# Optimization experiments

Hardware: AMD Instinct MI355X
Metric: run time of the kernel (lower is better)

The kernel has to match this reference:

```python
import jax, jax.numpy as jnp
import numpy as np

TOPK = 4  # constructor default topk=4


def setup_inputs() -> dict:
    key = jax.random.key(0)
    k_x, k_a, k_b, k_w, k_bias = jax.random.split(key, 5)
    b, s, h, j, a, r = 4, 2048, 2048, 2048, 64, 16
    x = jax.random.normal(k_x, (b, s, h), dtype=jnp.float32)
    A = jax.random.normal(k_a, (a, r, h), dtype=jnp.float32) * 0.02   # adapter down-proj bank
    B = jax.random.normal(k_b, (a, j, r), dtype=jnp.float32) * 0.02   # adapter up-proj bank
    W = jax.random.normal(k_w, (j, h), dtype=jnp.float32) * 0.02      # base Linear weight
    bias = jax.random.normal(k_bias, (j,), dtype=jnp.float32) * 0.02  # base Linear bias
    return {"x": x, "A": A, "B": B, "W": W, "bias": bias}


def reference(x, A, B, W, bias):
    # vecs: per-adapter low-rank projections of each token. [b,s,a,r]
    vecs = jnp.einsum('arh,bsh->bsar', A, x)
    # routing score = L2 norm over rank dim. [b,s,a]
    arrows = jnp.linalg.norm(vecs, axis=-1)
    # top-k adapters per token -> uniform 1/topk routing weights (scatter of a constant,
    # so no gradient flows through the routing weights, matching torch semantics).
    _, idx = jax.lax.top_k(arrows, TOPK)                     # [b,s,topk]
    routes = jax.nn.one_hot(idx, arrows.shape[-1], dtype=x.dtype).sum(-2) / TOPK  # [b,s,a]
    # weighted combine of selected adapter vecs. [b,s,r]
    v = jnp.einsum('bsa,bsar->bsr', routes, vecs)
    # delta = (routes-weighted B) applied to v; contract over a then r without
    # materializing the [b,s,j,r] intermediate. [b,s,j]
    delta = jnp.einsum('bsa,ajr,bsr->bsj', routes, B, v)
    base = jnp.einsum('bsh,jh->bsj', x, W) + bias
    return base + delta
```

## Files before the change

### kernel.cpp

```cpp
#include <hip/hip_runtime.h>
#include <hip/hip_bf16.h>
#include <stdint.h>

#define TOKENS 8192
#define H 2048
#define JDIM 2048
#define NADAPT 64
#define RANK 16
#define KG 1024
#define KTOT 3072
#define NT2 48

typedef __bf16 v8bf __attribute__((ext_vector_type(8)));
typedef float v4f __attribute__((ext_vector_type(4)));
typedef unsigned short us8 __attribute__((ext_vector_type(8)));
typedef unsigned short us4 __attribute__((ext_vector_type(4)));

__device__ __forceinline__ unsigned short f2bf(float f) {
  union { __bf16 b; unsigned short u; } c; c.b = (__bf16)f; return c.u;
}
__device__ __forceinline__ float bf2f(unsigned short u) {
  union { unsigned int u; float f; } c; c.u = ((unsigned int)u) << 16; return c.f;
}

__device__ __forceinline__ us8 pack8(float4 a, float4 b) {
  us8 r;
  r[0]=f2bf(a.x); r[1]=f2bf(a.y); r[2]=f2bf(a.z); r[3]=f2bf(a.w);
  r[4]=f2bf(b.x); r[5]=f2bf(b.y); r[6]=f2bf(b.z); r[7]=f2bf(b.w);
  return r;
}

__device__ __forceinline__ void split8(float4 a, float4 b, us8& h, us8& l) {
  float v[8] = {a.x, a.y, a.z, a.w, b.x, b.y, b.z, b.w};
  #pragma unroll
  for (int i = 0; i < 8; ++i) {
    h[i] = f2bf(v[i]);
    l[i] = f2bf(v[i] - bf2f(h[i]));
  }
}

__global__ void cast_x_split_kernel(const float* __restrict__ x,
                                    unsigned short* __restrict__ XG,
                                    unsigned short* __restrict__ XLO) {
  int idx = blockIdx.x * 256 + threadIdx.x;
  int row = idx >> 8;
  int cg  = idx & 255;
  const float4* s = (const float4*)(x + ((size_t)row << 11) + ((size_t)cg << 3));
  float4 a = s[0], b = s[1];
  us8 h, l;
  split8(a, b, h, l);
  *(us8*)(XG  + (size_t)row * KTOT + ((size_t)cg << 3)) = h;
  *(us8*)(XLO + (size_t)row * H    + ((size_t)cg << 3)) = l;
}

__global__ void cast_a_split_kernel(const float* __restrict__ A,
                                    unsigned short* __restrict__ Ahi,
                                    unsigned short* __restrict__ Alo) {
  int idx = blockIdx.x * 256 + threadIdx.x;
  int row = idx >> 8;
  int cg  = idx & 255;
  const float4* s = (const float4*)(A + ((size_t)row << 11) + ((size_t)cg << 3));
  float4 a = s[0], b = s[1];
  us8 h, l;
  split8(a, b, h, l);
  *(us8*)(Ahi + (size_t)row * H + ((size_t)cg << 3)) = h;
  *(us8*)(Alo + (size_t)row * H + ((size_t)cg << 3)) = l;
}

__global__ void cast2048_kernel(const float* __restrict__ src,
                                unsigned short* __restrict__ dst, int dstld) {
  int idx = blockIdx.x * 256 + threadIdx.x;
  int row = idx >> 8;
  int cg  = idx & 255;
  const float4* s = (const float4*)(src + ((size_t)row << 11) + ((size_t)cg << 3));
  float4 a = s[0], b = s[1];
  *(us8*)(dst + (size_t)row * dstld + ((size_t)cg << 3)) = pack8(a, b);
}

__global__ void cast_b_kernel(const float* __restrict__ Bsrc,
                              unsigned short* __restrict__ WB) {
  int idx = blockIdx.x * 256 + threadIdx.x;
  int a = idx >> 11, j = idx & 2047;
  const float4* s = (const float4*)(Bsrc + (((size_t)a << 11) + j) * RANK);
  float4 f0 = s[0], f1 = s[1], f2 = s[2], f3 = s[3];
  us8* d = (us8*)(WB + (size_t)j * KTOT + H + a * RANK);
  d[0] = pack8(f0, f1);
  d[1] = pack8(f2, f3);
}

__global__ void route_kernel(const float* __restrict__ vecs,
                             unsigned short* __restrict__ XG) {
  __shared__ float vsh[4][16];
  int wave = threadIdx.x >> 6, lane = threadIdx.x & 63;
  int t = blockIdx.x * 4 + wave;
  const float* vrow = vecs + (size_t)t * KG;
  const float4* vp = (const float4*)(vrow + lane * RANK);
  float4 q0 = vp[0], q1 = vp[1], q2 = vp[2], q3 = vp[3];
  float ss = q0.x*q0.x + q0.y*q0.y + q0.z*q0.z + q0.w*q0.w
           + q1.x*q1.x + q1.y*q1.y + q1.z*q1.z + q1.w*q1.w
           + q2.x*q2.x + q2.y*q2.y + q2.z*q2.z + q2.w*q2.w
           + q3.x*q3.x + q3.y*q3.y + q3.z*q3.z + q3.w*q3.w;
  float arr = ss;
  int sel[4];
  #pragma unroll
  for (int k = 0; k < 4; ++k) {
    float m = arr; int mi = lane;
    #pragma unroll
    for (int o = 32; o > 0; o >>= 1) {
      float om = __shfl_xor(m, o);
      int oi  = __shfl_xor(mi, o);
      if (om > m || (om == m && oi < mi)) { m = om; mi = oi; }
    }
    sel[k] = mi;
    if (lane == mi) arr = -3.0e38f;
  }
  if (lane < 16) {
    float s = vrow[sel[0]*RANK + lane] + vrow[sel[1]*RANK + lane]
            + vrow[sel[2]*RANK + lane] + vrow[sel[3]*RANK + lane];
    vsh[wave][lane] = 0.0625f * s;
  }
  __syncthreads();
  bool on = (lane == sel[0]) | (lane == sel[1]) | (lane == sel[2]) | (lane == sel[3]);
  us8 lo, hi;
  #pragma unroll
  for (int r = 0; r < 8; ++r) lo[r] = on ? f2bf(vsh[wave][r])     : (unsigned short)0;
  #pragma unroll
  for (int r = 0; r < 8; ++r) hi[r] = on ? f2bf(vsh[wave][r + 8]) : (unsigned short)0;
  us8* d = (us8*)(XG + (size_t)t * KTOT + H + lane * RANK);
  d[0] = lo; d[1] = hi;
}

__device__ __forceinline__ void gload_lds16(const void* gsrc, void* ldst) {
  __builtin_amdgcn_global_load_lds(
      (const __attribute__((address_space(1))) unsigned int*)gsrc,
      (__attribute__((address_space(3))) unsigned int*)ldst, 16, 0, 0);
}

__global__ __launch_bounds__(256, 2) void gemm1_kernel(
    const unsigned short* __restrict__ Xhi,
    const unsigned short* __restrict__ Xlo,
    const unsigned short* __restrict__ Ahi,
    const unsigned short* __restrict__ Alo,
    float* __restrict__ C) {
  __shared__ unsigned short AsH[128 * 32];
  __shared__ unsigned short AsL[128 * 32];
  __shared__ unsigned short BsH[128 * 32];
  __shared__ unsigned short BsL[128 * 32];
  const int tid = threadIdx.x;
  const int lane = tid & 63, wave = tid >> 6;
  const int wr = wave >> 1, wc = wave & 1;
  const int bm = blockIdx.x, bn = blockIdx.y;

  v4f acc[4][4];
  #pragma unroll
  for (int i = 0; i < 4; ++i)
    #pragma unroll
    for (int j = 0; j < 4; ++j)
      acc[i][j] = (v4f){0.f, 0.f, 0.f, 0.f};

  const unsigned short* XhiB = Xhi + (size_t)(bm * 128) * KTOT;
  const unsigned short* XloB = Xlo + (size_t)(bm * 128) * H;
  const unsigned short* AhiB = Ahi + (size_t)(bn * 128) * H;
  const unsigned short* AloB = Alo + (size_t)(bn * 128) * H;

  const int rA = lane & 15;
  const int kkx = (((lane >> 4) ^ ((rA >> 1) & 3)) << 3);

  for (int k0 = 0; k0 < H; k0 += 32) {
    #pragma unroll
    for (int rnd = 0; rnd < 2; ++rnd) {
      int e = rnd * 256 + tid;
      int r = e >> 2;
      int c8 = (((e & 3) ^ ((e >> 3) & 3)) << 3);
      gload_lds16(XhiB + (size_t)r * KTOT + k0 + c8, (char*)AsH + (size_t)e * 16);
      gload_lds16(XloB + (size_t)r * H    + k0 + c8, (char*)AsL + (size_t)e * 16);
      gload_lds16(AhiB + (size_t)r * H    + k0 + c8, (char*)BsH + (size_t)e * 16);
      gload_lds16(AloB + (size_t)r * H    + k0 + c8, (char*)BsL + (size_t)e * 16);
    }
    __syncthreads();
    v8bf ah[4], al[4], bh[4], bl[4];
    #pragma unroll
    for (int i = 0; i < 4; ++i) {
      ah[i] = *(const v8bf*)&AsH[(wr * 64 + i * 16 + rA) * 32 + kkx];
      al[i] = *(const v8bf*)&AsL[(wr * 64 + i * 16 + rA) * 32 + kkx];
    }
    #pragma unroll
    for (int j = 0; j < 4; ++j) {
      bh[j] = *(const v8bf*)&BsH[(wc * 64 + j * 16 + rA) * 32 + kkx];
      bl[j] = *(const v8bf*)&BsL[(wc * 64 + j * 16 + rA) * 32 + kkx];
    }
    #pragma unroll
    for (int i = 0; i < 4; ++i)
      #pragma unroll
      for (int j = 0; j < 4; ++j) {
        acc[i][j] = __builtin_amdgcn_mfma_f32_16x16x32_bf16(ah[i], bh[j], acc[i][j], 0, 0, 0);
        acc[i][j] = __builtin_amdgcn_mfma_f32_16x16x32_bf16(ah[i], bl[j], acc[i][j], 0, 0, 0);
        acc[i][j] = __builtin_amdgcn_mfma_f32_16x16x32_bf16(al[i], bh[j], acc[i][j], 0, 0, 0);
      }
    __syncthreads();
  }

  const int rowbase = bm * 128 + wr * 64;
  const int colbase = bn * 128 + wc * 64;
  #pragma unroll
  for (int i = 0; i < 4; ++i) {
    int r0 = rowbase + i * 16 + ((lane >> 4) << 2);
    #pragma unroll
    for (int j = 0; j < 4; ++j) {
      int col = colbase + j * 16 + (lane & 15);
      #pragma unroll
      for (int q = 0; q < 4; ++q)
        C[(size_t)(r0 + q) * KG + col] = acc[i][j][q];
    }
  }
}

#define BAR() asm volatile("s_waitcnt lgkmcnt(0)\n\ts_barrier" ::: "memory")
#define VM8() asm volatile("s_waitcnt vmcnt(8)" ::: "memory")

#define STAGE(regionUS, panel, kelem) do {                                        \
  gload_lds16((panel) + aoff0 + (kelem), (char*)(regionUS) + tid * 16);           \
  gload_lds16((panel) + aoff1 + (kelem), (char*)(regionUS) + 8192 + tid * 16);    \
} while (0)

#define PHASE(mh, RAr, RBr, ISSUE, DOVM) do {                                     \
  if ((mh) == 0) {                                                                \
    _Pragma("unroll")                                                             \
    for (int j = 0; j < 4; ++j)                                                   \
      bfr[j] = *(const v8bf*)((const char*)(RBr) + bbyte + j * 1024);             \
  }                                                                               \
  _Pragma("unroll")                                                               \
  for (int i = 0; i < 4; ++i)                                                     \
    af[i] = *(const v8bf*)((const char*)(RAr) + abyte + ((mh)*4 + i) * 1024);     \
  ISSUE;                                                                          \
  BAR();                                                                          \
  __builtin_amdgcn_s_setprio(1);                                                  \
  _Pragma("unroll")                                                               \
  for (int i = 0; i < 4; ++i)                                                     \
    _Pragma("unroll")                                                             \
    for (int j = 0; j < 4; ++j)                                                   \
      acc[(mh)*4 + i][j] = __builtin_amdgcn_mfma_f32_16x16x32_bf16(               \
          af[i], bfr[j], acc[(mh)*4 + i][j], 0, 0, 0);                            \
  __builtin_amdgcn_s_setprio(0);                                                  \
  DOVM;                                                                           \
  BAR();                                                                          \
} while (0)

__global__ __launch_bounds__(512, 1) void gemm2_8ph_kernel(
    const unsigned short* __restrict__ Xg, const unsigned short* __restrict__ Wb,
    float* __restrict__ C, const float* __restrict__ bias) {
  __shared__ unsigned short lds[65536];
  const int tid = threadIdx.x;
  const int lane = tid & 63, wid = tid >> 6;
  const int wr = wid >> 2, wc = wid & 3;
  const int rA = lane & 15, grp = lane >> 4;
  const int grpx = (grp ^ ((rA >> 1) & 3)) << 4;

  const int bid = blockIdx.x;
  const int bn = bid & 7, bm = bid >> 3;

  const unsigned short* Ap = Xg + (size_t)(bm * 256) * KTOT;
  const unsigned short* Bp = Wb + (size_t)(bn * 256) * KTOT;

  const int srow = tid >> 2;
  const int scol = ((tid & 3) ^ ((tid >> 3) & 3)) << 3;
  const size_t aoff0 = (size_t)srow * KTOT + scol;
  const size_t aoff1 = (size_t)(srow + 128) * KTOT + scol;

  unsigned short* A0k0 = lds;
  unsigned short* A0k1 = lds + 8192;
  unsigned short* B0k0 = lds + 16384;
  unsigned short* B0k1 = lds + 24576;
  unsigned short* A1k0 = lds + 32768;
  unsigned short* A1k1 = lds + 40960;
  unsigned short* B1k0 = lds + 49152;
  unsigned short* B1k1 = lds + 57344;

  const int abyte = (wr * 128 + rA) * 64 + grpx;
  const int bbyte = (wc * 64 + rA) * 64 + grpx;

  v4f acc[8][4];
  #pragma unroll
  for (int i = 0; i < 8; ++i)
    #pragma unroll
    for (int j = 0; j < 4; ++j)
      acc[i][j] = (v4f){0.f, 0.f, 0.f, 0.f};
  v8bf af[4], bfr[4];

  STAGE(A0k0, Ap, 0);
  STAGE(B0k0, Bp, 0);
  STAGE(A0k1, Ap, 32);
  STAGE(B0k1, Bp, 32);
  STAGE(A1k0, Ap, 64);
  STAGE(B1k0, Bp, 64);
  VM8();
  BAR();

  #pragma unroll 1
  for (int t = 0; t < NT2; t += 2) {
    const int k1a = (t + 1) * 64 + 32;
    const int k0a = (t + 2 < NT2 ? t + 2 : NT2 - 1) * 64;
    const int k1b = (t + 2 < NT2 ? t + 2 : NT2 - 1) * 64 + 32;
    const int k0b = (t + 3 < NT2 ? t + 3 : NT2 - 1) * 64;
    PHASE(0, A0k0, B0k0, STAGE(A1k1, Ap, k1a), ((void)0));
    PHASE(1, A0k0, B0k0, STAGE(B1k1, Bp, k1a), VM8());
    PHASE(0, A0k1, B0k1, STAGE(A0k0, Ap, k0a), ((void)0));
    PHASE(1, A0k1, B0k1, STAGE(B0k0, Bp, k0a), VM8());
    PHASE(0, A1k0, B1k0, STAGE(A0k1, Ap, k1b), ((void)0));
    PHASE(1, A1k0, B1k0, STAGE(B0k1, Bp, k1b), VM8());
    PHASE(0, A1k1, B1k1, STAGE(A1k0, Ap, k0b), ((void)0));
    PHASE(1, A1k1, B1k1, STAGE(B1k0, Bp, k0b), VM8());
  }

  const int row0 = bm * 256 + wr * 128 + (grp << 2);
  const int col0 = bn * 256 + wc * 64 + rA;
  float bv[4];
  #pragma unroll
  for (int j = 0; j < 4; ++j) bv[j] = bias[col0 + j * 16];
  #pragma unroll
  for (int mi = 0; mi < 8; ++mi)
    #pragma unroll
    for (int j = 0; j < 4; ++j)
      #pragma unroll
      for (int q = 0; q < 4; ++q)
        C[(size_t)(row0 + mi * 16 + q) * JDIM + col0 + j * 16] = acc[mi][j][q] + bv[j];
}

extern "C" void kernel_launch(void* const* d_in, const int* in_sizes, int n_in,
                              void* d_out, int out_size, void* d_ws, size_t ws_size,
                              hipStream_t stream) {
  const float* x    = (const float*)d_in[0];
  const float* A    = (const float*)d_in[1];
  const float* Bb   = (const float*)d_in[2];
  const float* W    = (const float*)d_in[3];
  const float* bias = (const float*)d_in[4];
  float* out = (float*)d_out;

  char* ws = (char*)d_ws;
  unsigned short* XG  = (unsigned short*)ws;
  unsigned short* WB  = (unsigned short*)(ws + (size_t)48 * 1024 * 1024);
  unsigned short* Ahi = (unsigned short*)(ws + (size_t)60 * 1024 * 1024);
  unsigned short* Alo = (unsigned short*)(ws + (size_t)64 * 1024 * 1024);
  float* vecs         = (float*)d_out;
  unsigned short* XLO = (unsigned short*)((char*)d_out + (size_t)32 * 1024 * 1024);

  cast_x_split_kernel<<<TOKENS, 256, 0, stream>>>(x, XG, XLO);
  cast_a_split_kernel<<<KG / 1, 256, 0, stream>>>(A, Ahi, Alo);
  cast2048_kernel<<<JDIM, 256, 0, stream>>>(W, WB, KTOT);
  cast_b_kernel<<<512, 256, 0, stream>>>(Bb, WB);

  gemm1_kernel<<<dim3(TOKENS / 128, KG / 128), 256, 0, stream>>>(
      XG, XLO, Ahi, Alo, vecs);

  route_kernel<<<TOKENS / 4, 256, 0, stream>>>(vecs, XG);

  gemm2_8ph_kernel<<<256, 512, 0, stream>>>(XG, WB, out, bias);
}
```

Measured before the change: 232.1 us.

## Rewrite routing GEMM as double-buffered 8-wave phased pipeline

Result: slower. 240.9 us (+3.8%).

```diff
diff --git a/kernel.cpp b/kernel.cpp
--- a/kernel.cpp
+++ b/kernel.cpp
@@ -10,6 +10,7 @@
 #define KG 1024
 #define KTOT 3072
 #define NT2 48
+#define NT1 64
 
 typedef __bf16 v8bf __attribute__((ext_vector_type(8)));
 typedef float v4f __attribute__((ext_vector_type(4)));
@@ -136,20 +137,93 @@
       (__attribute__((address_space(3))) unsigned int*)ldst, 16, 0, 0);
 }
 
-__global__ __launch_bounds__(256, 2) void gemm1_kernel(
+#define BAR() asm volatile("s_waitcnt lgkmcnt(0)\n\ts_barrier" ::: "memory")
+#define VM2() asm volatile("s_waitcnt vmcnt(2)" ::: "memory")
+#define VM3() asm volatile("s_waitcnt vmcnt(3)" ::: "memory")
+#define VM8() asm volatile("s_waitcnt vmcnt(8)" ::: "memory")
+#define P1() __builtin_amdgcn_s_setprio(1)
+#define P0() __builtin_amdgcn_s_setprio(0)
+
+#define MM1(mi, xf, bv) do {                                                   \
+  acc[mi][0] = __builtin_amdgcn_mfma_f32_16x16x32_bf16(xf, bv[0], acc[mi][0], 0, 0, 0); \
+  acc[mi][1] = __builtin_amdgcn_mfma_f32_16x16x32_bf16(xf, bv[1], acc[mi][1], 0, 0, 0); \
+  acc[mi][2] = __builtin_amdgcn_mfma_f32_16x16x32_bf16(xf, bv[2], acc[mi][2], 0, 0, 0); \
+  acc[mi][3] = __builtin_amdgcn_mfma_f32_16x16x32_bf16(xf, bv[3], acc[mi][3], 0, 0, 0); \
+} while (0)
+
+#define LD1(off) (*(const v8bf*)(Lb + (off)))
+
+#define S_XH1(b, kel) gload_lds16(XhB + (size_t)srow * KTOT + (kel) + scol, Lb + (b)*49152 + tid*16)
+#define S_XH2(b, kel) gload_lds16(XhB + (size_t)(srow + 128) * KTOT + (kel) + scol, Lb + (b)*49152 + 8192 + tid*16)
+#define S_XL1(b, kel) gload_lds16(XlB + (size_t)srow * H + (kel) + scol, Lb + (b)*49152 + 16384 + tid*16)
+#define S_XL2(b, kel) gload_lds16(XlB + (size_t)(srow + 128) * H + (kel) + scol, Lb + (b)*49152 + 24576 + tid*16)
+#define S_AH1(b, kel) gload_lds16(AhB + (size_t)srow * H + (kel) + scol, Lb + (b)*49152 + 32768 + tid*16)
+#define S_AL1(b, kel) gload_lds16(AlB + (size_t)srow * H + (kel) + scol, Lb + (b)*49152 + 40960 + tid*16)
+
+#define TILE1(c, n, kn) do {                                                   \
+                                                         \
+  xh[0] = LD1((c)*49152 + abyte);                                              \
+  xh[1] = LD1((c)*49152 + abyte + 1024);                                       \
+  ah[0] = LD1((c)*49152 + 32768 + bbyte);                                      \
+  ah[1] = LD1((c)*49152 + 32768 + bbyte + 1024);                               \
+  ah[2] = LD1((c)*49152 + 32768 + bbyte + 2048);                               \
+  ah[3] = LD1((c)*49152 + 32768 + bbyte + 3072);                               \
+  S_XH1(n, kn);                                                                \
+  BAR(); P1(); MM1(0, xh[0], ah); MM1(1, xh[1], ah); P0(); BAR();              \
+                                                         \
+  xh[2] = LD1((c)*49152 + abyte + 2048);                                       \
+  xh[3] = LD1((c)*49152 + abyte + 3072);                                       \
+  S_XH2(n, kn);                                                                \
+  BAR(); P1(); MM1(2, xh[2], ah); MM1(3, xh[3], ah); P0(); VM2(); BAR();       \
+                                                         \
+  al[0] = LD1((c)*49152 + 40960 + bbyte);                                      \
+  al[1] = LD1((c)*49152 + 40960 + bbyte + 1024);                               \
+  al[2] = LD1((c)*49152 + 40960 + bbyte + 2048);                               \
+  al[3] = LD1((c)*49152 + 40960 + bbyte + 3072);                               \
+  S_AH1(n, kn);                                                                \
+  BAR(); P1(); MM1(0, xh[0], al); MM1(1, xh[1], al); P0(); BAR();              \
+                                                         \
+  S_XL1(n, kn);                                                                \
+  BAR(); P1(); MM1(2, xh[2], al); MM1(3, xh[3], al); P0(); BAR();              \
+                                                         \
+  xl[0] = LD1((c)*49152 + 16384 + abyte);                                      \
+  xl[1] = LD1((c)*49152 + 16384 + abyte + 1024);                               \
+  S_XL2(n, kn);                                                                \
+  BAR(); P1(); MM1(0, xl[0], ah); MM1(1, xl[1], ah); P0(); BAR();              \
+                                                         \
+  xl[2] = LD1((c)*49152 + 16384 + abyte + 2048);                               \
+  xl[3] = LD1((c)*49152 + 16384 + abyte + 3072);                               \
+  S_AL1(n, kn);                                                                \
+  BAR(); P1(); MM1(2, xl[2], ah); MM1(3, xl[3], ah); P0(); VM3(); BAR();       \
+} while (0)
+
+__global__ __launch_bounds__(512, 1) void gemm1_8ph_kernel(
     const unsigned short* __restrict__ Xhi,
     const unsigned short* __restrict__ Xlo,
     const unsigned short* __restrict__ Ahi,
     const unsigned short* __restrict__ Alo,
     float* __restrict__ C) {
-  __shared__ unsigned short AsH[128 * 32];
-  __shared__ unsigned short AsL[128 * 32];
-  __shared__ unsigned short BsH[128 * 32];
-  __shared__ unsigned short BsL[128 * 32];
+  __shared__ char Ls[98304];
+  char* Lb = Ls;
   const int tid = threadIdx.x;
-  const int lane = tid & 63, wave = tid >> 6;
-  const int wr = wave >> 1, wc = wave & 1;
-  const int bm = blockIdx.x, bn = blockIdx.y;
+  const int lane = tid & 63, wid = tid >> 6;
+  const int wr = wid >> 1, wc = wid & 1;
+  const int rA = lane & 15, grp = lane >> 4;
+  const int grpx = (grp ^ ((rA >> 1) & 3)) << 4;
+
+  const int bid = blockIdx.x;
+  const int bn = bid & 7, bm = bid >> 3;
+
+  const unsigned short* XhB = Xhi + (size_t)(bm * 256) * KTOT;
+  const unsigned short* XlB = Xlo + (size_t)(bm * 256) * H;
+  const unsigned short* AhB = Ahi + (size_t)(bn * 128) * H;
+  const unsigned short* AlB = Alo + (size_t)(bn * 128) * H;
+
+  const int srow = tid >> 2;
+  const int scol = ((tid & 3) ^ ((tid >> 3) & 3)) << 3;
+
+  const int abyte = (wr * 64 + rA) * 64 + grpx;
+  const int bbyte = (wc * 64 + rA) * 64 + grpx;
 
   v4f acc[4][4];
   #pragma unroll
@@ -157,66 +231,29 @@
     #pragma unroll
     for (int j = 0; j < 4; ++j)
       acc[i][j] = (v4f){0.f, 0.f, 0.f, 0.f};
-
-  const unsigned short* XhiB = Xhi + (size_t)(bm * 128) * KTOT;
-  const unsigned short* XloB = Xlo + (size_t)(bm * 128) * H;
-  const unsigned short* AhiB = Ahi + (size_t)(bn * 128) * H;
-  const unsigned short* AloB = Alo + (size_t)(bn * 128) * H;
-
-  const int rA = lane & 15;
-  const int kkx = (((lane >> 4) ^ ((rA >> 1) & 3)) << 3);
-
-  for (int k0 = 0; k0 < H; k0 += 32) {
-    #pragma unroll
-    for (int rnd = 0; rnd < 2; ++rnd) {
-      int e = rnd * 256 + tid;
-      int r = e >> 2;
-      int c8 = (((e & 3) ^ ((e >> 3) & 3)) << 3);
-      gload_lds16(XhiB + (size_t)r * KTOT + k0 + c8, (char*)AsH + (size_t)e * 16);
-      gload_lds16(XloB + (size_t)r * H    + k0 + c8, (char*)AsL + (size_t)e * 16);
-      gload_lds16(AhiB + (size_t)r * H    + k0 + c8, (char*)BsH + (size_t)e * 16);
-      gload_lds16(AloB + (size_t)r * H    + k0 + c8, (char*)BsL + (size_t)e * 16);
-    }
-    __syncthreads();
-    v8bf ah[4], al[4], bh[4], bl[4];
-    #pragma unroll
-    for (int i = 0; i < 4; ++i) {
-      ah[i] = *(const v8bf*)&AsH[(wr * 64 + i * 16 + rA) * 32 + kkx];
-      al[i] = *(const v8bf*)&AsL[(wr * 64 + i * 16 + rA) * 32 + kkx];
-    }
-    #pragma unroll
-    for (int j = 0; j < 4; ++j) {
-      bh[j] = *(const v8bf*)&BsH[(wc * 64 + j * 16 + rA) * 32 + kkx];
-      bl[j] = *(const v8bf*)&BsL[(wc * 64 + j * 16 + rA) * 32 + kkx];
-    }
-    #pragma unroll
-    for (int i = 0; i < 4; ++i)
-      #pragma unroll
-      for (int j = 0; j < 4; ++j) {
-        acc[i][j] = __builtin_amdgcn_mfma_f32_16x16x32_bf16(ah[i], bh[j], acc[i][j], 0, 0, 0);
-        acc[i][j] = __builtin_amdgcn_mfma_f32_16x16x32_bf16(ah[i], bl[j], acc[i][j], 0, 0, 0);
-        acc[i][j] = __builtin_amdgcn_mfma_f32_16x16x32_bf16(al[i], bh[j], acc[i][j], 0, 0, 0);
-      }
-    __syncthreads();
-  }
-
-  const int rowbase = bm * 128 + wr * 64;
-  const int colbase = bn * 128 + wc * 64;
-  #pragma unroll
-  for (int i = 0; i < 4; ++i) {
-    int r0 = rowbase + i * 16 + ((lane >> 4) << 2);
-    #pragma unroll
-    for (int j = 0; j < 4; ++j) {
-      int col = colbase + j * 16 + (lane & 15);
+  v8bf xh[4], xl[4], ah[4], al[4];
+
+  S_XH1(0, 0); S_XH2(0, 0); S_AH1(0, 0); S_XL1(0, 0); S_XL2(0, 0); S_AL1(0, 0);
+  VM3(); BAR();
+
+  #pragma unroll 1
+  for (int t = 0; t < NT1; t += 2) {
+    const int ka = (t + 1) * 32;
+    const int kb = (t + 2 < NT1 ? t + 2 : NT1 - 1) * 32;
+    TILE1(0, 1, ka);
+    TILE1(1, 0, kb);
+  }
+
+  const int row0 = bm * 256 + wr * 64 + (grp << 2);
+  const int col0 = bn * 128 + wc * 64 + rA;
+  #pragma unroll
+  for (int mi = 0; mi < 4; ++mi)
+    #pragma unroll
+    for (int j = 0; j < 4; ++j)
       #pragma unroll
       for (int q = 0; q < 4; ++q)
-        C[(size_t)(r0 + q) * KG + col] = acc[i][j][q];
-    }
-  }
-}
-
-#define BAR() asm volatile("s_waitcnt lgkmcnt(0)\n\ts_barrier" ::: "memory")
-#define VM8() asm volatile("s_waitcnt vmcnt(8)" ::: "memory")
+        C[(size_t)(row0 + mi * 16 + q) * KG + col0 + j * 16] = acc[mi][j][q];
+}
 
 #define STAGE(regionUS, panel, kelem) do {                                        \
   gload_lds16((panel) + aoff0 + (kelem), (char*)(regionUS) + tid * 16);           \
@@ -234,14 +271,14 @@
     af[i] = *(const v8bf*)((const char*)(RAr) + abyte + ((mh)*4 + i) * 1024);     \
   ISSUE;                                                                          \
   BAR();                                                                          \
-  __builtin_amdgcn_s_setprio(1);                                                  \
+  P1();                                                                           \
   _Pragma("unroll")                                                               \
   for (int i = 0; i < 4; ++i)                                                     \
     _Pragma("unroll")                                                             \
     for (int j = 0; j < 4; ++j)                                                   \
       acc[(mh)*4 + i][j] = __builtin_amdgcn_mfma_f32_16x16x32_bf16(               \
           af[i], bfr[j], acc[(mh)*4 + i][j], 0, 0, 0);                            \
-  __builtin_amdgcn_s_setprio(0);                                                  \
+  P0();                                                                           \
   DOVM;                                                                           \
   BAR();                                                                          \
 } while (0)
@@ -345,12 +382,11 @@
   unsigned short* XLO = (unsigned short*)((char*)d_out + (size_t)32 * 1024 * 1024);
 
   cast_x_split_kernel<<<TOKENS, 256, 0, stream>>>(x, XG, XLO);
-  cast_a_split_kernel<<<KG / 1, 256, 0, stream>>>(A, Ahi, Alo);
+  cast_a_split_kernel<<<KG, 256, 0, stream>>>(A, Ahi, Alo);
   cast2048_kernel<<<JDIM, 256, 0, stream>>>(W, WB, KTOT);
   cast_b_kernel<<<512, 256, 0, stream>>>(Bb, WB);
 
-  gemm1_kernel<<<dim3(TOKENS / 128, KG / 128), 256, 0, stream>>>(
-      XG, XLO, Ahi, Alo, vecs);
+  gemm1_8ph_kernel<<<256, 512, 0, stream>>>(XG, XLO, Ahi, Alo, vecs);
 
   route_kernel<<<TOKENS / 4, 256, 0, stream>>>(vecs, XG);
 
```
